# Performance work log

Measured on AMD Instinct MI355X. Metric: run time of the kernel, lower is better.

The kernel has to match this reference:

```python
import jax, jax.numpy as jnp
import numpy as np

# Scaled-down LLaMA-style decoder with per-layer memory K/V prefix (tokenmix2 Decoder)
L, D, H, Dh, F, V = 2, 4096, 32, 128, 8192, 8192
B, S, M = 1, 1024, 512
EPS = 1e-5
ROPE_BASE = 10000.0


def setup_inputs() -> dict:
    key = jax.random.key(0)
    ks = jax.random.split(key, 16)
    sd = D ** -0.5
    sf = F ** -0.5
    n = lambda k, shape, s: (jax.random.normal(k, shape, jnp.float32) * s)
    return {
        "input_ids": jax.random.randint(ks[0], (B, S), 0, V),
        "memory": jax.random.normal(ks[1], (L, B, M, D), jnp.float32),
        "embed": n(ks[2], (V, D), sd),
        "Wq": n(ks[3], (L, D, D), sd),
        "Wk": n(ks[4], (L, D, D), sd),
        "Wv": n(ks[5], (L, D, D), sd),
        "Wo": n(ks[6], (L, D, D), sd),
        "Wg": n(ks[7], (L, F, D), sd),
        "Wu": n(ks[8], (L, F, D), sd),
        "Wd": n(ks[9], (L, D, F), sf),
        "Wmk": n(ks[10], (L, D, D), sd),
        "Wmv": n(ks[11], (L, D, D), sd),
        "ln1": jnp.ones((L, D), jnp.float32),
        "ln2": jnp.ones((L, D), jnp.float32),
        "normw": jnp.ones((D,), jnp.float32),
        "lm_head": n(ks[12], (V, D), sd),
    }


def _rms(x, w):
    return x * jax.lax.rsqrt(jnp.mean(x * x, axis=-1, keepdims=True) + EPS) * w


def _rot_half(x):
    x1, x2 = jnp.split(x, 2, axis=-1)
    return jnp.concatenate([-x2, x1], axis=-1)


def _rope_tables(n_pos):
    inv_freq = 1.0 / (ROPE_BASE ** (jnp.arange(0, Dh, 2, dtype=jnp.float32) / Dh))
    ang = jnp.arange(n_pos, dtype=jnp.float32)[:, None] * inv_freq[None, :]
    emb = jnp.concatenate([ang, ang], axis=-1)  # [n_pos, Dh]
    return jnp.cos(emb), jnp.sin(emb)


def reference(input_ids, memory, embed, Wq, Wk, Wv, Wo, Wg, Wu, Wd, Wmk, Wmv,
              ln1, ln2, normw, lm_head):
    h = embed[input_ids]                                   # [B,S,D]
    cos, sin = _rope_tables(M + S)                         # memory tokens sit at positions 0..M
    cos_k, sin_k = cos[None, None], sin[None, None]        # [1,1,M+S,Dh]
    cos_q, sin_q = cos[None, None, M:], sin[None, None, M:]  # queries at positions M..M+S
    qpos = jnp.arange(M, M + S)
    kpos = jnp.arange(M + S)
    mask = qpos[:, None] >= kpos[None, :]                  # causal incl. full memory prefix
    scale = Dh ** -0.5

    def heads(x, T):
        return x.reshape(B, T, H, Dh).transpose(0, 2, 1, 3)  # [B,H,T,Dh]

    for l in range(L):
        x = _rms(h, ln1[l])
        q = heads(x @ Wq[l].T, S)
        k = heads(x @ Wk[l].T, S)
        v = heads(x @ Wv[l].T, S)
        mk = heads(memory[l] @ Wmk[l].T, M)
        mv = heads(memory[l] @ Wmv[l].T, M)
        K = jnp.concatenate([mk, k], axis=2)               # [B,H,M+S,Dh]
        Vv = jnp.concatenate([mv, v], axis=2)
        q = q * cos_q + _rot_half(q) * sin_q
        K = K * cos_k + _rot_half(K) * sin_k
        scores = jnp.einsum('bhqd,bhkd->bhqk', q, K) * scale
        scores = jnp.where(mask, scores, jnp.float32(-1e30))
        p = jax.nn.softmax(scores, axis=-1)
        o = jnp.einsum('bhqk,bhkd->bhqd', p, Vv)
        o = o.transpose(0, 2, 1, 3).reshape(B, S, D)
        h = h + o @ Wo[l].T
        x = _rms(h, ln2[l])
        h = h + (jax.nn.silu(x @ Wg[l].T) * (x @ Wu[l].T)) @ Wd[l].T

    h = _rms(h, normw)
    logits = (h @ lm_head.T).astype(jnp.float32)           # [B,S,V]
    return logits
```

## Files before the change

kernel.cpp:

```cpp
#include <hip/hip_runtime.h>
#include <hip/hip_bf16.h>

typedef unsigned int uint;
typedef unsigned short u16;

#define D_ 4096
#define H_ 32
#define DH 128
#define F_ 8192
#define V_ 8192
#define S_ 1024
#define M_ 512
#define L_ 2
#define KV_ (M_ + S_)

typedef __attribute__((ext_vector_type(8))) short s16x8;
typedef __attribute__((ext_vector_type(4))) float f32x4;
typedef __attribute__((ext_vector_type(4))) u16 u16x4;

__device__ __forceinline__ u16 f2bf(float f) {
    uint u = __float_as_uint(f);
    u += 0x7FFFu + ((u >> 16) & 1u);
    return (u16)(u >> 16);
}
__device__ __forceinline__ float bf2f(u16 h) {
    return __uint_as_float(((uint)h) << 16);
}
__device__ __forceinline__ uint cvt_pk_bf16(float a, float b) {
    uint r;
    asm volatile("v_cvt_pk_bf16_f32 %0, %1, %2" : "=v"(r) : "v"(a), "v"(b));
    return r;
}
__device__ __forceinline__ void gload_lds16(const void* g, void* l) {
    __builtin_amdgcn_global_load_lds(
        (const __attribute__((address_space(1))) unsigned int*)g,
        (__attribute__((address_space(3))) unsigned int*)l, 16, 0, 0);
}

__global__ void k_embed(const int* __restrict__ ids, const float* __restrict__ embed,
                        float* __restrict__ h) {
    int row = blockIdx.x;
    const float4* src = (const float4*)(embed + (size_t)ids[row] * D_);
    float4* dst = (float4*)(h + (size_t)row * D_);
    for (int i = threadIdx.x; i < D_ / 4; i += 256) dst[i] = src[i];
}

__global__ __launch_bounds__(256) void k_rms(const float* __restrict__ hin,
                                             const float* __restrict__ w,
                                             u16* __restrict__ out) {
    int row = blockIdx.x, t = threadIdx.x;
    const float4* src = (const float4*)(hin + (size_t)row * D_);
    float4 v[4];
    float ss = 0.f;
#pragma unroll
    for (int i = 0; i < 4; ++i) {
        v[i] = src[t + 256 * i];
        ss += v[i].x * v[i].x + v[i].y * v[i].y + v[i].z * v[i].z + v[i].w * v[i].w;
    }
#pragma unroll
    for (int off = 32; off; off >>= 1) ss += __shfl_xor(ss, off);
    __shared__ float red[4];
    if ((t & 63) == 0) red[t >> 6] = ss;
    __syncthreads();
    float tot = red[0] + red[1] + red[2] + red[3];
    float sc = rsqrtf(tot * (1.0f / D_) + 1e-5f);
    const float4* wp = (const float4*)w;
    u16x4* op = (u16x4*)(out + (size_t)row * D_);
#pragma unroll
    for (int i = 0; i < 4; ++i) {
        float4 wv = wp[t + 256 * i];
        u16x4 o;
        o[0] = f2bf(v[i].x * sc * wv.x);
        o[1] = f2bf(v[i].y * sc * wv.y);
        o[2] = f2bf(v[i].z * sc * wv.z);
        o[3] = f2bf(v[i].w * sc * wv.w);
        op[t + 256 * i] = o;
    }
}

__global__ void k_cvt(const float* __restrict__ src, u16* __restrict__ dst, int n4) {
    int i = blockIdx.x * 256 + threadIdx.x;
    if (i < n4) {
        float4 v = ((const float4*)src)[i];
        u16x4 o;
        o[0] = f2bf(v.x); o[1] = f2bf(v.y); o[2] = f2bf(v.z); o[3] = f2bf(v.w);
        ((u16x4*)dst)[i] = o;
    }
}

__global__ void k_ropetab(float* __restrict__ tab) {
    int pos = blockIdx.x, i = threadIdx.x;
    float invf = powf(10000.0f, -(float)i * (1.0f / 64.0f));
    float ang = (float)pos * invf;
    tab[(size_t)pos * 128 + i * 2] = cosf(ang);
    tab[(size_t)pos * 128 + i * 2 + 1] = sinf(ang);
}

__global__ __launch_bounds__(256) void k_rope(u16* __restrict__ buf,
                                              const float* __restrict__ tab, int pos0) {
    int row = blockIdx.x, t = threadIdx.x;
    const float2* tp = (const float2*)(tab + (size_t)(pos0 + row) * 128);
    u16* p = buf + (size_t)row * D_;
#pragma unroll
    for (int j = 0; j < 8; ++j) {
        int pid = t + 256 * j;
        int hd = pid >> 6, i = pid & 63;
        float2 cs = tp[i];
        int base = hd * 128 + i;
        float v0 = bf2f(p[base]), v1 = bf2f(p[base + 64]);
        p[base] = f2bf(v0 * cs.x - v1 * cs.y);
        p[base + 64] = f2bf(v1 * cs.x + v0 * cs.y);
    }
}

__global__ __launch_bounds__(256) void k_transpose(const u16* __restrict__ src,
                                                   u16* __restrict__ dst) {
    __shared__ u16 tile[64][66];
    int tc = blockIdx.x * 64;
    int tr = blockIdx.y * 64;
    int t = threadIdx.x;
    int c = t & 63, r0 = t >> 6;
#pragma unroll
    for (int i = 0; i < 16; ++i) {
        int r = r0 + i * 4;
        tile[r][c] = src[(size_t)(tr + r) * D_ + tc + c];
    }
    __syncthreads();
#pragma unroll
    for (int i = 0; i < 16; ++i) {
        int r = r0 + i * 4;
        dst[(size_t)(tc + r) * KV_ + tr + c] = tile[c][r];
    }
}

struct GemmBatch {
    const u16* A[5];
    const float* B[5];
    void* O[5];
    int mrows[5];
    int koff[5];
    float* aux;
};

template <int EPI>
__global__ __launch_bounds__(256) void k_gemm(GemmBatch P, int Nn, int Kstep, int Kfull) {
    int z = blockIdx.z;
    size_t bm = blockIdx.y, bn = blockIdx.x;
    if ((int)(bm * 128) >= P.mrows[z]) return;
    const u16* A = P.A[z];
    const float* Bw = P.B[z];
    int koff = P.koff[z];

    __shared__ __align__(16) u16 As[2][128 * 64];
    __shared__ __align__(16) u16 Bs[2][128 * 64];
    int tid = threadIdx.x;
    int lane = tid & 63, wid = tid >> 6;
    int l16 = lane & 15, lh = lane >> 4;
    int wm = (wid >> 1) * 64, wn = (wid & 1) * 64;

    const u16* pA[4];
    const float* pB[4];
    int ldsAo[4], bso[4];
#pragma unroll
    for (int i = 0; i < 4; ++i) {
        int c = tid + 256 * i;
        int r = c >> 3, s = c & 7;
        pA[i] = A + (size_t)(bm * 128 + r) * Kfull + koff + s * 8;
        pB[i] = Bw + (size_t)(bn * 128 + r) * Kfull + koff + s * 8;
        ldsAo[i] = c * 8;
        bso[i] = r * 64 + ((s ^ (r & 7)) * 8);
    }

    f32x4 acc[4][4];
#pragma unroll
    for (int i = 0; i < 4; ++i)
#pragma unroll
        for (int j = 0; j < 4; ++j)
#pragma unroll
            for (int e = 0; e < 4; ++e) acc[i][j][e] = 0.f;

    float4 br[8];
    auto issueA = [&](int p, int k0) {
#pragma unroll
        for (int i = 0; i < 4; ++i)
            gload_lds16(pA[i] + k0, &As[p][0] + ldsAo[i]);
    };
    auto issueB = [&](int k0) {
#pragma unroll
        for (int i = 0; i < 4; ++i) {
            br[2 * i] = *(const float4*)(pB[i] + k0);
            br[2 * i + 1] = *(const float4*)(pB[i] + k0 + 4);
        }
    };
    auto cvtwrite = [&](int p) {
#pragma unroll
        for (int i = 0; i < 4; ++i) {
            uint4 w;
            w.x = cvt_pk_bf16(br[2 * i].x, br[2 * i].y);
            w.y = cvt_pk_bf16(br[2 * i].z, br[2 * i].w);
            w.z = cvt_pk_bf16(br[2 * i + 1].x, br[2 * i + 1].y);
            w.w = cvt_pk_bf16(br[2 * i + 1].z, br[2 * i + 1].w);
            *(uint4*)(&Bs[p][bso[i]]) = w;
        }
    };
    auto compute = [&](int p) {
#pragma unroll
        for (int kk = 0; kk < 2; ++kk) {
            int sidx = kk * 4 + lh;
            s16x8 af[4], bf4[4];
#pragma unroll
            for (int mi = 0; mi < 4; ++mi)
                af[mi] = *(const s16x8*)(&As[p][(wm + mi * 16 + l16) * 64 + sidx * 8]);
#pragma unroll
            for (int ni = 0; ni < 4; ++ni) {
                int r = wn + ni * 16 + l16;
                bf4[ni] = *(const s16x8*)(&Bs[p][r * 64 + ((sidx ^ (r & 7)) * 8)]);
            }
#pragma unroll
            for (int mi = 0; mi < 4; ++mi)
#pragma unroll
                for (int ni = 0; ni < 4; ++ni)
                    acc[mi][ni] = __builtin_amdgcn_mfma_f32_16x16x32_bf16(
                        af[mi], bf4[ni], acc[mi][ni], 0, 0, 0);
        }
    };

    int nt = Kstep >> 6;
    issueA(0, 0);
    issueB(0);
    cvtwrite(0);
    __syncthreads();
    int p = 0;
    for (int t = 0; t < nt; ++t) {
        bool pre = (t + 1 < nt);
        if (pre) {
            issueA(p ^ 1, (t + 1) << 6);
            issueB((t + 1) << 6);
        }
        compute(p);
        if (pre) cvtwrite(p ^ 1);
        __syncthreads();
        p ^= 1;
    }

    void* Oo = P.O[z];
#pragma unroll
    for (int mi = 0; mi < 4; ++mi) {
#pragma unroll
        for (int ni = 0; ni < 4; ++ni) {
#pragma unroll
            for (int r = 0; r < 4; ++r) {
                int grow = (int)bm * 128 + wm + mi * 16 + lh * 4 + r;
                int gcol = (int)bn * 128 + wn + ni * 16 + l16;
                size_t idx = (size_t)grow * Nn + gcol;
                float v = acc[mi][ni][r];
                if constexpr (EPI == 0) {
                    ((u16*)Oo)[idx] = f2bf(v);
                } else if constexpr (EPI == 1) {
                    ((float*)Oo)[idx] = v;
                } else if constexpr (EPI == 3) {
                    float g = P.aux[idx];
                    float sg = g / (1.0f + __expf(-g));
                    ((u16*)Oo)[idx] = f2bf(sg * v);
                } else {
                    atomicAdd((float*)Oo + idx, v);
                }
            }
        }
    }
}

__global__ __launch_bounds__(64) void k_attn(const u16* __restrict__ Qb,
                                             const u16* __restrict__ Kb,
                                             const u16* __restrict__ VT,
                                             u16* __restrict__ Ob) {
    int qt = blockIdx.x, hd = blockIdx.y;
    int lane = threadIdx.x, l16 = lane & 15, lh = lane >> 4;
    __shared__ __align__(16) float Pl[16 * 36];

    s16x8 qf[4];
#pragma unroll
    for (int c = 0; c < 4; ++c)
        qf[c] = *(const s16x8*)(Qb + (size_t)(qt * 16 + l16) * D_ + hd * DH + c * 32 + lh * 8);

    f32x4 o[8];
#pragma unroll
    for (int dc = 0; dc < 8; ++dc)
#pragma unroll
        for (int e = 0; e < 4; ++e) o[dc][e] = 0.f;
    float m[4], lsum[4];
#pragma unroll
    for (int r = 0; r < 4; ++r) { m[r] = -1e30f; lsum[r] = 0.f; }

    const float scale = 0.08838834764831845f;
    int qbase = M_ + qt * 16;
    int nkb = (M_ + qt * 16 + 16 + 31) >> 5;

    for (int kb = 0; kb < nkb; ++kb) {
        f32x4 s0, s1;
#pragma unroll
        for (int e = 0; e < 4; ++e) { s0[e] = 0.f; s1[e] = 0.f; }
#pragma unroll
        for (int c = 0; c < 4; ++c) {
            s16x8 kf0 = *(const s16x8*)(Kb + (size_t)(kb * 32 + l16) * D_ + hd * DH + c * 32 + lh * 8);
            s16x8 kf1 = *(const s16x8*)(Kb + (size_t)(kb * 32 + 16 + l16) * D_ + hd * DH + c * 32 + lh * 8);
            s0 = __builtin_amdgcn_mfma_f32_16x16x32_bf16(qf[c], kf0, s0, 0, 0, 0);
            s1 = __builtin_amdgcn_mfma_f32_16x16x32_bf16(qf[c], kf1, s1, 0, 0, 0);
        }
        int kp0 = kb * 32 + l16, kp1 = kp0 + 16;
        float pm[4];
#pragma unroll
        for (int r = 0; r < 4; ++r) {
            int qp = qbase + lh * 4 + r;
            float v0 = s0[r] * scale; if (kp0 > qp) v0 = -1e30f;
            float v1 = s1[r] * scale; if (kp1 > qp) v1 = -1e30f;
            s0[r] = v0; s1[r] = v1;
            pm[r] = fmaxf(v0, v1);
        }
#pragma unroll
        for (int r = 0; r < 4; ++r) {
#pragma unroll
            for (int off = 8; off; off >>= 1) pm[r] = fmaxf(pm[r], __shfl_xor(pm[r], off));
        }
        float alpha[4];
#pragma unroll
        for (int r = 0; r < 4; ++r) {
            float mn = fmaxf(m[r], pm[r]);
            alpha[r] = __expf(m[r] - mn);
            m[r] = mn;
            float p0 = __expf(s0[r] - mn), p1 = __expf(s1[r] - mn);
            s0[r] = p0; s1[r] = p1;
            float t = p0 + p1;
#pragma unroll
            for (int off = 8; off; off >>= 1) t += __shfl_xor(t, off);
            lsum[r] = lsum[r] * alpha[r] + t;
        }
#pragma unroll
        for (int r = 0; r < 4; ++r) {
            Pl[(lh * 4 + r) * 36 + l16] = s0[r];
            Pl[(lh * 4 + r) * 36 + 16 + l16] = s1[r];
        }
        __syncthreads();
        s16x8 pf;
        {
            const f32x4* pp = (const f32x4*)(Pl + l16 * 36 + lh * 8);
            f32x4 a = pp[0], b = pp[1];
            pf[0] = (short)f2bf(a[0]); pf[1] = (short)f2bf(a[1]);
            pf[2] = (short)f2bf(a[2]); pf[3] = (short)f2bf(a[3]);
            pf[4] = (short)f2bf(b[0]); pf[5] = (short)f2bf(b[1]);
            pf[6] = (short)f2bf(b[2]); pf[7] = (short)f2bf(b[3]);
        }
        __syncthreads();
#pragma unroll
        for (int dc = 0; dc < 8; ++dc) {
#pragma unroll
            for (int r = 0; r < 4; ++r) o[dc][r] *= alpha[r];
        }
#pragma unroll
        for (int dc = 0; dc < 8; ++dc) {
            s16x8 vf = *(const s16x8*)(VT + (size_t)(hd * DH + dc * 16 + l16) * KV_ + kb * 32 + lh * 8);
            o[dc] = __builtin_amdgcn_mfma_f32_16x16x32_bf16(pf, vf, o[dc], 0, 0, 0);
        }
    }
#pragma unroll
    for (int dc = 0; dc < 8; ++dc) {
#pragma unroll
        for (int r = 0; r < 4; ++r) {
            float val = o[dc][r] / lsum[r];
            Ob[(size_t)(qt * 16 + lh * 4 + r) * D_ + hd * DH + dc * 16 + l16] = f2bf(val);
        }
    }
}

extern "C" void kernel_launch(void* const* d_in, const int* in_sizes, int n_in,
                              void* d_out, int out_size, void* d_ws, size_t ws_size,
                              hipStream_t stream) {
    const int* ids = (const int*)d_in[0];
    const float* memory = (const float*)d_in[1];
    const float* embed = (const float*)d_in[2];
    const float* Wq = (const float*)d_in[3];
    const float* Wk = (const float*)d_in[4];
    const float* Wv = (const float*)d_in[5];
    const float* Wo = (const float*)d_in[6];
    const float* Wg = (const float*)d_in[7];
    const float* Wu = (const float*)d_in[8];
    const float* Wd = (const float*)d_in[9];
    const float* Wmk = (const float*)d_in[10];
    const float* Wmv = (const float*)d_in[11];
    const float* ln1 = (const float*)d_in[12];
    const float* ln2 = (const float*)d_in[13];
    const float* normw = (const float*)d_in[14];
    const float* lm = (const float*)d_in[15];

    char* ws = (char*)d_ws;
    float* h   = (float*)(ws + 0x0000000);
    u16* xb    = (u16*)(ws + 0x1000000);
    float* tab = (float*)(ws + 0x1800000);
    u16* memb  = (u16*)(ws + 0x1900000);
    u16* Qb    = (u16*)(ws + 0x1E00000);
    u16* Kb    = (u16*)(ws + 0x2600000);
    u16* Vb    = (u16*)(ws + 0x3200000);
    u16* VT    = (u16*)(ws + 0x3E00000);
    u16* Ob    = (u16*)(ws + 0x4A00000);
    float* Gbuf = (float*)(ws + 0x1E00000);
    u16* tb     = (u16*)(ws + 0x3E00000);

    k_embed<<<S_, 256, 0, stream>>>(ids, embed, h);
    k_ropetab<<<KV_, 64, 0, stream>>>(tab);

    for (int l = 0; l < L_; ++l) {
        const float* Wq_l = Wq + (size_t)l * D_ * D_;
        const float* Wk_l = Wk + (size_t)l * D_ * D_;
        const float* Wv_l = Wv + (size_t)l * D_ * D_;
        const float* Wo_l = Wo + (size_t)l * D_ * D_;
        const float* Wmk_l = Wmk + (size_t)l * D_ * D_;
        const float* Wmv_l = Wmv + (size_t)l * D_ * D_;
        const float* Wg_l = Wg + (size_t)l * (size_t)F_ * D_;
        const float* Wu_l = Wu + (size_t)l * (size_t)F_ * D_;
        const float* Wd_l = Wd + (size_t)l * (size_t)D_ * F_;

        k_rms<<<S_, 256, 0, stream>>>(h, ln1 + l * D_, xb);
        k_cvt<<<(M_ * D_ / 4 + 255) / 256, 256, 0, stream>>>(
            memory + (size_t)l * M_ * D_, memb, M_ * D_ / 4);

        GemmBatch g1{};
        g1.A[0] = xb;   g1.B[0] = Wq_l;  g1.O[0] = Qb;                    g1.mrows[0] = S_;
        g1.A[1] = xb;   g1.B[1] = Wk_l;  g1.O[1] = Kb + (size_t)M_ * D_;  g1.mrows[1] = S_;
        g1.A[2] = xb;   g1.B[2] = Wv_l;  g1.O[2] = Vb + (size_t)M_ * D_;  g1.mrows[2] = S_;
        g1.A[3] = memb; g1.B[3] = Wmk_l; g1.O[3] = Kb;                    g1.mrows[3] = M_;
        g1.A[4] = memb; g1.B[4] = Wmv_l; g1.O[4] = Vb;                    g1.mrows[4] = M_;
        k_gemm<0><<<dim3(D_ / 128, S_ / 128, 5), 256, 0, stream>>>(g1, D_, D_, D_);

        k_rope<<<S_, 256, 0, stream>>>(Qb, tab, M_);
        k_rope<<<KV_, 256, 0, stream>>>(Kb, tab, 0);
        k_transpose<<<dim3(D_ / 64, KV_ / 64), 256, 0, stream>>>(Vb, VT);
        k_attn<<<dim3(S_ / 16, H_), 64, 0, stream>>>(Qb, Kb, VT, Ob);

        GemmBatch g2{};
        g2.A[0] = Ob; g2.B[0] = Wo_l; g2.O[0] = h; g2.mrows[0] = S_; g2.koff[0] = 0;
        g2.A[1] = Ob; g2.B[1] = Wo_l; g2.O[1] = h; g2.mrows[1] = S_; g2.koff[1] = 2048;
        k_gemm<4><<<dim3(D_ / 128, S_ / 128, 2), 256, 0, stream>>>(g2, D_, 2048, D_);

        k_rms<<<S_, 256, 0, stream>>>(h, ln2 + l * D_, xb);
        GemmBatch g3{};
        g3.A[0] = xb; g3.B[0] = Wg_l; g3.O[0] = Gbuf; g3.mrows[0] = S_;
        k_gemm<1><<<dim3(F_ / 128, S_ / 128, 1), 256, 0, stream>>>(g3, F_, D_, D_);
        GemmBatch g4{};
        g4.A[0] = xb; g4.B[0] = Wu_l; g4.O[0] = tb; g4.mrows[0] = S_; g4.aux = Gbuf;
        k_gemm<3><<<dim3(F_ / 128, S_ / 128, 1), 256, 0, stream>>>(g4, F_, D_, D_);
        GemmBatch g5{};
        g5.A[0] = tb; g5.B[0] = Wd_l; g5.O[0] = h; g5.mrows[0] = S_; g5.koff[0] = 0;
        g5.A[1] = tb; g5.B[1] = Wd_l; g5.O[1] = h; g5.mrows[1] = S_; g5.koff[1] = 4096;
        k_gemm<4><<<dim3(D_ / 128, S_ / 128, 2), 256, 0, stream>>>(g5, D_, 4096, F_);
    }

    k_rms<<<S_, 256, 0, stream>>>(h, normw, xb);
    GemmBatch g6{};
    g6.A[0] = xb; g6.B[0] = lm; g6.O[0] = (float*)d_out; g6.mrows[0] = S_;
    k_gemm<1><<<dim3(V_ / 128, S_ / 128, 1), 256, 0, stream>>>(g6, V_, D_, D_);
}
```

Measured before the change: 1.863 ms.

## Replace double-buffered LDS GEMM pipeline with single buffer and register prefetch

Cuts the GEMM kernel's shared-memory tiles from two stages to one (32KB instead of 64KB), so more blocks can be resident per CU. B is still prefetched into registers one step ahead, but the A tile is now loaded straight into LDS within each iteration and waited on before compute. Each K-step now needs two barriers, and the A global-to-LDS load is no longer overlapped with MFMA work.

```diff
diff --git a/kernel.cpp b/kernel.cpp
--- a/kernel.cpp
+++ b/kernel.cpp
@@ -151,8 +151,8 @@
     const float* Bw = P.B[z];
     int koff = P.koff[z];
 
-    __shared__ __align__(16) u16 As[2][128 * 64];
-    __shared__ __align__(16) u16 Bs[2][128 * 64];
+    __shared__ __align__(16) u16 As[128 * 64];
+    __shared__ __align__(16) u16 Bs[128 * 64];
     int tid = threadIdx.x;
     int lane = tid & 63, wid = tid >> 6;
     int l16 = lane & 15, lh = lane >> 4;
@@ -180,19 +180,19 @@
             for (int e = 0; e < 4; ++e) acc[i][j][e] = 0.f;
 
     float4 br[8];
-    auto issueA = [&](int p, int k0) {
+    auto issueA = [&](int k0) {
 #pragma unroll
         for (int i = 0; i < 4; ++i)
-            gload_lds16(pA[i] + k0, &As[p][0] + ldsAo[i]);
+            gload_lds16(pA[i] + k0, &As[0] + ldsAo[i]);
     };
-    auto issueB = [&](int k0) {
+    auto loadB = [&](int k0) {
 #pragma unroll
         for (int i = 0; i < 4; ++i) {
             br[2 * i] = *(const float4*)(pB[i] + k0);
             br[2 * i + 1] = *(const float4*)(pB[i] + k0 + 4);
         }
     };
-    auto cvtwrite = [&](int p) {
+    auto cvtwriteB = [&]() {
 #pragma unroll
         for (int i = 0; i < 4; ++i) {
             uint4 w;
@@ -200,21 +200,21 @@
             w.y = cvt_pk_bf16(br[2 * i].z, br[2 * i].w);
             w.z = cvt_pk_bf16(br[2 * i + 1].x, br[2 * i + 1].y);
             w.w = cvt_pk_bf16(br[2 * i + 1].z, br[2 * i + 1].w);
-            *(uint4*)(&Bs[p][bso[i]]) = w;
+            *(uint4*)(&Bs[bso[i]]) = w;
         }
     };
-    auto compute = [&](int p) {
+    auto compute = [&]() {
 #pragma unroll
         for (int kk = 0; kk < 2; ++kk) {
             int sidx = kk * 4 + lh;
             s16x8 af[4], bf4[4];
 #pragma unroll
             for (int mi = 0; mi < 4; ++mi)
-                af[mi] = *(const s16x8*)(&As[p][(wm + mi * 16 + l16) * 64 + sidx * 8]);
+                af[mi] = *(const s16x8*)(&As[(wm + mi * 16 + l16) * 64 + sidx * 8]);
 #pragma unroll
             for (int ni = 0; ni < 4; ++ni) {
                 int r = wn + ni * 16 + l16;
-                bf4[ni] = *(const s16x8*)(&Bs[p][r * 64 + ((sidx ^ (r & 7)) * 8)]);
+                bf4[ni] = *(const s16x8*)(&Bs[r * 64 + ((sidx ^ (r & 7)) * 8)]);
             }
 #pragma unroll
             for (int mi = 0; mi < 4; ++mi)
@@ -226,21 +226,14 @@
     };
 
     int nt = Kstep >> 6;
-    issueA(0, 0);
-    issueB(0);
-    cvtwrite(0);
-    __syncthreads();
-    int p = 0;
+    loadB(0);
     for (int t = 0; t < nt; ++t) {
-        bool pre = (t + 1 < nt);
-        if (pre) {
-            issueA(p ^ 1, (t + 1) << 6);
-            issueB((t + 1) << 6);
-        }
-        compute(p);
-        if (pre) cvtwrite(p ^ 1);
+        issueA(t << 6);
+        cvtwriteB();
+        if (t + 1 < nt) loadB((t + 1) << 6);
         __syncthreads();
-        p ^= 1;
+        compute();
+        __syncthreads();
     }
 
     void* Oo = P.O[z];
```

After: 1.891 ms. No clear change (+1.5%).
